# Optimization experiments

Hardware: AMD Instinct MI355X
Metric: run time of the kernel (lower is better)

## Reference

```python
import jax, jax.numpy as jnp
import numpy as np

T, N, E = 4, 4096, 65536
XD, HD, ZD = 256, 256, 64
EPS = 1e-10


def setup_inputs() -> dict:
    key = jax.random.key(0)
    ks = jax.random.split(key, 30)
    rn = lambda k, sh, s=0.05: jax.random.normal(k, sh, dtype=jnp.float32) * s
    inp = {
        "x": rn(ks[0], (T, N, XD), 1.0),
        "edge_idx": jax.random.randint(ks[1], (T, 2, E), 0, N, dtype=jnp.int32),
        "adj": jax.random.bernoulli(ks[2], 0.005, (T, N, N)).astype(jnp.float32),
        "eps_noise": jax.random.normal(ks[3], (T, N, ZD), dtype=jnp.float32),
        "h0": jnp.zeros((1, N, HD), jnp.float32),
        # phi_x / phi_z (Linear+ReLU)
        "phi_x_w": rn(ks[4], (XD, HD)), "phi_x_b": jnp.zeros((HD,), jnp.float32),
        "phi_z_w": rn(ks[5], (ZD, HD)), "phi_z_b": jnp.zeros((HD,), jnp.float32),
        # encoder GCNs
        "enc_w": rn(ks[6], (2 * HD, HD)), "enc_b": jnp.zeros((HD,), jnp.float32),
        "enc_mean_w": rn(ks[7], (HD, ZD)), "enc_mean_b": jnp.zeros((ZD,), jnp.float32),
        "enc_std_w": rn(ks[8], (HD, ZD)), "enc_std_b": jnp.zeros((ZD,), jnp.float32),
        # prior MLPs
        "prior_w": rn(ks[9], (HD, HD)), "prior_b": jnp.zeros((HD,), jnp.float32),
        "prior_mean_w": rn(ks[10], (HD, ZD)), "prior_mean_b": jnp.zeros((ZD,), jnp.float32),
        "prior_std_w": rn(ks[11], (HD, ZD)), "prior_std_b": jnp.zeros((ZD,), jnp.float32),
        # graph-GRU GCNs (bias=False, n_layers=1; x-input is cat[phi_x, phi_z] -> 2*HD)
        "gru_xz_w": rn(ks[12], (2 * HD, HD)), "gru_hz_w": rn(ks[13], (HD, HD)),
        "gru_xr_w": rn(ks[14], (2 * HD, HD)), "gru_hr_w": rn(ks[15], (HD, HD)),
        "gru_xh_w": rn(ks[16], (2 * HD, HD)), "gru_hh_w": rn(ks[17], (HD, HD)),
    }
    return inp


def _gcn(xf, src, dst, W, b):
    """GCNConv: sym-normalized (A + I) aggregation, then bias. Returns pre-activation."""
    h = xf @ W                                             # [N, out]
    deg = 1.0 + jax.ops.segment_sum(jnp.ones(src.shape[0], xf.dtype), dst, num_segments=N)
    dinv = jax.lax.rsqrt(deg)                              # [N]
    norm = dinv[src] * dinv[dst]                           # [E]
    agg = jax.ops.segment_sum(h[src] * norm[:, None], dst, num_segments=N)
    agg = agg + (dinv * dinv)[:, None] * h                 # self-loop term
    if b is not None:
        agg = agg + b
    return agg


def reference(x, edge_idx, adj, eps_noise, h0,
              phi_x_w, phi_x_b, phi_z_w, phi_z_b,
              enc_w, enc_b, enc_mean_w, enc_mean_b, enc_std_w, enc_std_b,
              prior_w, prior_b, prior_mean_w, prior_mean_b, prior_std_w, prior_std_b,
              gru_xz_w, gru_hz_w, gru_xr_w, gru_hr_w, gru_xh_w, gru_hh_w):
    relu, sp, sig = jax.nn.relu, jax.nn.softplus, jax.nn.sigmoid
    h = h0                                                  # [1, N, HD]
    kld = jnp.float32(0.0)
    nll = jnp.float32(0.0)
    enc_means, prior_means = [], []
    nn_f = jnp.float32(N * N)
    for t in range(T):
        src, dst = edge_idx[t, 0], edge_idx[t, 1]
        phi_x_t = relu(x[t] @ phi_x_w + phi_x_b)                       # [N, HD]
        enc_in = jnp.concatenate([phi_x_t, h[-1]], axis=1)             # [N, 2HD]
        enc_t = relu(_gcn(enc_in, src, dst, enc_w, enc_b))
        enc_mean_t = _gcn(enc_t, src, dst, enc_mean_w, enc_mean_b)     # act = identity
        enc_std_t = sp(_gcn(enc_t, src, dst, enc_std_w, enc_std_b))
        prior_t = relu(h[-1] @ prior_w + prior_b)
        prior_mean_t = prior_t @ prior_mean_w + prior_mean_b
        prior_std_t = sp(prior_t @ prior_std_w + prior_std_b)
        z_t = eps_noise[t] * enc_std_t + enc_mean_t                    # reparameterize
        phi_z_t = relu(z_t @ phi_z_w + phi_z_b)
        dec_t = sig(z_t @ z_t.T)                                       # [N, N] decode
        # graph-GRU step (n_layers = 1, bias=False)
        gin = jnp.concatenate([phi_x_t, phi_z_t], axis=1)              # [N, 2HD]
        z_g = sig(_gcn(gin, src, dst, gru_xz_w, None) + _gcn(h[0], src, dst, gru_hz_w, None))
        r_g = sig(_gcn(gin, src, dst, gru_xr_w, None) + _gcn(h[0], src, dst, gru_hr_w, None))
        h_tilde = jnp.tanh(_gcn(gin, src, dst, gru_xh_w, None)
                           + _gcn(r_g * h[0], src, dst, gru_hh_w, None))
        h = (z_g * h[0] + (1.0 - z_g) * h_tilde)[None]                 # [1, N, HD]
        # KLD (faithful to _kld_gauss, including its sign convention)
        s1, s2 = enc_std_t + EPS, prior_std_t + EPS
        kld_el = (2.0 * jnp.log(s2) - 2.0 * jnp.log(s1)
                  - (s1 * s1 + (enc_mean_t - prior_mean_t) ** 2) / (s2 * s2) + 1.0)
        kld = kld + (0.5 / N) * jnp.mean(jnp.sum(kld_el, axis=0))
        # NLL (faithful quirk: BCE-with-logits applied to sigmoid output dec_t)
        a = adj[t]
        tsum = jnp.sum(a)
        posw = (nn_f - tsum) / tsum
        norm = nn_f / ((nn_f - tsum) * 2.0)
        bce = posw * a * sp(-dec_t) + (1.0 - a) * sp(dec_t)
        nll = nll + norm * jnp.mean(bce)
        enc_means.append(enc_mean_t)
        prior_means.append(prior_mean_t)
    return kld, nll, jnp.stack(enc_means), jnp.stack(prior_means), h
```

## Files before the change

kernel.cpp:

```cpp
#include <hip/hip_runtime.h>
#include <hip/hip_bf16.h>

#define T_STEPS 4
#define N 4096
#define E 65536
#define XD 256
#define HD 256
#define ZD 64

typedef __hip_bfloat16 bf16;
typedef __attribute__((ext_vector_type(8))) short short8;
typedef __attribute__((ext_vector_type(4))) float f32x4;

__device__ __forceinline__ float b2f(bf16 v){ return __bfloat162float(v); }
__device__ __forceinline__ bf16 f2b(float v){ return __float2bfloat16(v); }
__device__ __forceinline__ short f2s(float v){ return __builtin_bit_cast(short, f2b(v)); }
__device__ __forceinline__ float bits2f(unsigned int s){ return __builtin_bit_cast(float, s << 16); }
__device__ __forceinline__ float s2f(short s){ return bits2f((unsigned int)(unsigned short)s); }
__device__ __forceinline__ float splus(float x){ return (x > 20.f) ? x : log1pf(expf(x)); }
__device__ __forceinline__ float sigm(float x){ return 1.f/(1.f + expf(-x)); }

__device__ __forceinline__ float ldI(const void* p, size_t i, int f){
  return f ? ((const float*)p)[i] : b2f(((const bf16*)p)[i]);
}
__device__ __forceinline__ void stO(void* p, size_t i, float v, int f){
  if (f) ((float*)p)[i] = v; else ((bf16*)p)[i] = f2b(v);
}
__device__ __forceinline__ void ld8b(const bf16* p, float v[8]){
  uint4 u = *(const uint4*)p;
  v[0]=bits2f(u.x & 0xffffu); v[1]=bits2f(u.x >> 16);
  v[2]=bits2f(u.y & 0xffffu); v[3]=bits2f(u.y >> 16);
  v[4]=bits2f(u.z & 0xffffu); v[5]=bits2f(u.z >> 16);
  v[6]=bits2f(u.w & 0xffffu); v[7]=bits2f(u.w >> 16);
}
__device__ __forceinline__ unsigned int pack2(float a, float b){
  return (unsigned int)(unsigned short)__builtin_bit_cast(unsigned short, f2b(a))
       | ((unsigned int)(unsigned short)__builtin_bit_cast(unsigned short, f2b(b)) << 16);
}

union SMem {
  struct { short As[64*40]; short Wt[64*40]; } g;
  struct { short Zi[64*72]; short Zj[64*72]; short Adj[64*72]; float red[256]; } z;
  struct { float msh[16*128]; } m;
  int sh[256];
  float red[256];
};

struct KP {
  const void *x, *adj, *eps, *h0;
  const int* ei;
  const void *phi_x_w, *phi_x_b, *phi_z_w, *phi_z_b;
  const void *enc_w, *enc_b, *enc_mean_w, *enc_mean_b, *enc_std_w, *enc_std_b;
  const void *prior_w, *prior_b, *prior_mean_w, *prior_mean_b, *prior_std_w, *prior_std_b;
  const void *gxz, *ghz, *gxr, *ghr, *gxh, *ghh;
  void* out;
  float* scal; int* dflag; float* dinv; int* offs; int* srcs; float* enorm; int* deg;
  float* h_prev; bf16* h_bf; bf16* phiXa; bf16* Tb1; bf16* Tb2;
  bf16* zbf; float* z_g; bf16* Gs1; bf16* Gsx; bf16* Gms; bf16* Gh2;
};

#define OUT_EM ((size_t)2)
#define OUT_PM ((size_t)(2 + (size_t)T_STEPS*N*ZD))
#define OUT_H  ((size_t)(2 + (size_t)2*T_STEPS*N*ZD))

__device__ void mfma_tile(SMem& sm, int tid, int f,
    const void* A1, int am1, int lda1, const void* A2, int am2, int lda2,
    int K1, int K, const void* W, int ldw, int wcol,
    const void* bias, int act, bf16* C, int ldc, int row0, int ccol0){
  int ar = tid >> 2, akk = (tid & 3)*8;
  int wk = tid >> 3, wn = (tid & 7)*8;
  int wave = tid >> 6, lane = tid & 63, m = lane & 15, kq = lane >> 4;
  f32x4 acc[4] = {};
  for (int k0 = 0; k0 < K; k0 += 32){
    const void* A; int am, lda, kb;
    if (k0 < K1){ A = A1; am = am1; lda = lda1; kb = k0; }
    else        { A = A2; am = am2; lda = lda2; kb = k0 - K1; }
    size_t aidx = (size_t)(row0 + ar)*lda + kb + akk;
    short8 av;
    if (am == 2 || (am == 1 && f == 0)){
      av = *(const short8*)((const short*)A + aidx);
    } else {
      const float* Af = (const float*)A;
      float4 u0 = *(const float4*)(Af + aidx);
      float4 u1 = *(const float4*)(Af + aidx + 4);
      av[0]=f2s(u0.x); av[1]=f2s(u0.y); av[2]=f2s(u0.z); av[3]=f2s(u0.w);
      av[4]=f2s(u1.x); av[5]=f2s(u1.y); av[6]=f2s(u1.z); av[7]=f2s(u1.w);
    }
    *(short8*)&sm.g.As[ar*40 + akk] = av;
    size_t wi = (size_t)(k0 + wk)*ldw + wcol + wn;
    short wv[8];
    if (f == 0){
      short8 t8 = *(const short8*)((const short*)W + wi);
      #pragma unroll
      for (int j = 0; j < 8; j++) wv[j] = t8[j];
    } else {
      const float* Wf = (const float*)W;
      float4 u0 = *(const float4*)(Wf + wi);
      float4 u1 = *(const float4*)(Wf + wi + 4);
      wv[0]=f2s(u0.x); wv[1]=f2s(u0.y); wv[2]=f2s(u0.z); wv[3]=f2s(u0.w);
      wv[4]=f2s(u1.x); wv[5]=f2s(u1.y); wv[6]=f2s(u1.z); wv[7]=f2s(u1.w);
    }
    #pragma unroll
    for (int j = 0; j < 8; j++){
      int nrow = wn + j;
      int col = (((wk >> 3) ^ ((nrow >> 3) & 3)) << 3) | (wk & 7);
      sm.g.Wt[nrow*40 + col] = wv[j];
    }
    __syncthreads();
    short8 afr = *(const short8*)&sm.g.As[(wave*16 + m)*40 + kq*8];
    #pragma unroll
    for (int t4 = 0; t4 < 4; t4++){
      int nb = t4*16 + m;
      short8 bfr = *(const short8*)&sm.g.Wt[nb*40 + ((kq ^ ((nb >> 3) & 3)) << 3)];
      acc[t4] = __builtin_amdgcn_mfma_f32_16x16x32_bf16(afr, bfr, acc[t4], 0, 0, 0);
    }
    __syncthreads();
  }
  #pragma unroll
  for (int t4 = 0; t4 < 4; t4++){
    int c = ccol0 + t4*16 + m;
    float bv = bias ? ldI(bias, wcol + t4*16 + m, f) : 0.f;
    #pragma unroll
    for (int reg = 0; reg < 4; reg++){
      int r = row0 + wave*16 + kq*4 + reg;
      float v = acc[t4][reg] + bv;
      if (act == 1) v = fmaxf(v, 0.f);
      C[(size_t)r*ldc + c] = f2b(v);
    }
  }
}

__device__ void dec_tile1(const KP& p, SMem& sm, int tid, int t, int u, int f){
  int i0 = (u >> 6)*64, j0 = (u & 63)*64;
  size_t aoff = (size_t)t*N*N;
  #pragma unroll
  for (int i = 0; i < 2; i++){
    int idx = tid + i*256;
    int r = idx >> 3, c = idx & 7;
    int col = ((c ^ ((r >> 3) & 3)) << 3);
    *(short8*)&sm.z.Zi[r*72 + col] = *(const short8*)((const short*)p.zbf + (size_t)(i0+r)*ZD + c*8);
    *(short8*)&sm.z.Zj[r*72 + col] = *(const short8*)((const short*)p.zbf + (size_t)(j0+r)*ZD + c*8);
  }
  {
    int row = tid >> 2, c0 = (tid & 3)*16;
    if (f){
      const float* ap = (const float*)p.adj + aoff + (size_t)(i0+row)*N + j0 + c0;
      short tmp[16];
      #pragma unroll
      for (int q = 0; q < 16; q += 4){
        float4 v = *(const float4*)(ap + q);
        tmp[q]=f2s(v.x); tmp[q+1]=f2s(v.y); tmp[q+2]=f2s(v.z); tmp[q+3]=f2s(v.w);
      }
      *(short8*)&sm.z.Adj[row*72 + c0]     = *(short8*)&tmp[0];
      *(short8*)&sm.z.Adj[row*72 + c0 + 8] = *(short8*)&tmp[8];
    } else {
      const short* ap = (const short*)p.adj + aoff + (size_t)(i0+row)*N + j0 + c0;
      *(short8*)&sm.z.Adj[row*72 + c0]     = *(const short8*)ap;
      *(short8*)&sm.z.Adj[row*72 + c0 + 8] = *(const short8*)(ap + 8);
    }
  }
  __syncthreads();
  int wave = tid >> 6, lane = tid & 63, m = lane & 15, kq = lane >> 4;
  int ra = wave*16 + m, sa = (ra >> 3) & 3;
  short8 a1 = *(const short8*)&sm.z.Zi[ra*72 + ((kq ^ sa) << 3)];
  short8 a2 = *(const short8*)&sm.z.Zi[ra*72 + (((kq+4) ^ sa) << 3)];
  f32x4 acc[4] = {};
  #pragma unroll
  for (int t4 = 0; t4 < 4; t4++){
    int rb = t4*16 + m, sb2 = (rb >> 3) & 3;
    short8 b1 = *(const short8*)&sm.z.Zj[rb*72 + ((kq ^ sb2) << 3)];
    short8 b2 = *(const short8*)&sm.z.Zj[rb*72 + (((kq+4) ^ sb2) << 3)];
    acc[t4] = __builtin_amdgcn_mfma_f32_16x16x32_bf16(a1, b1, acc[t4], 0, 0, 0);
    acc[t4] = __builtin_amdgcn_mfma_f32_16x16x32_bf16(a2, b2, acc[t4], 0, 0, 0);
  }
  float lts = 0.f, lP = 0.f, lQ = 0.f;
  #pragma unroll
  for (int t4 = 0; t4 < 4; t4++){
    int lj = t4*16 + m;
    #pragma unroll
    for (int reg = 0; reg < 4; reg++){
      int li = wave*16 + kq*4 + reg;
      float av = s2f(sm.z.Adj[li*72 + lj]);
      float dec = sigm(acc[t4][reg]);
      lts += av;
      lQ += (1.f - av)*log1pf(expf(dec));
      if (av != 0.f) lP += av*log1pf(expf(-dec));
    }
  }
  __syncthreads();
  sm.z.red[tid] = lts; __syncthreads();
  for (int o = 128; o > 0; o >>= 1){ if (tid < o) sm.z.red[tid] += sm.z.red[tid+o]; __syncthreads(); }
  if (tid == 0) atomicAdd(p.scal + 8 + t, sm.z.red[0]);
  __syncthreads();
  sm.z.red[tid] = lP; __syncthreads();
  for (int o = 128; o > 0; o >>= 1){ if (tid < o) sm.z.red[tid] += sm.z.red[tid+o]; __syncthreads(); }
  if (tid == 0) atomicAdd(p.scal + 12 + t, sm.z.red[0]);
  __syncthreads();
  sm.z.red[tid] = lQ; __syncthreads();
  for (int o = 128; o > 0; o >>= 1){ if (tid < o) sm.z.red[tid] += sm.z.red[tid+o]; __syncthreads(); }
  if (tid == 0) atomicAdd(p.scal + 16 + t, sm.z.red[0]);
}

__global__ __launch_bounds__(256) void setup0_k(KP p){
  int gb = blockIdx.x, tid = threadIdx.x;
  if (gb == 0){ if (tid < 64) p.scal[tid] = 0.f; }
  else if (gb == 1){
    if (tid == 0){
      const unsigned short* u = (const unsigned short*)p.x;
      int big = 0;
      for (int i = 0; i < 256; i++){ int e = (u[i] >> 7) & 0xFF; if (e >= 134) big++; }
      *p.dflag = (big > 16) ? 1 : 0;
    }
  } else {
    p.deg[(gb-2)*256 + tid] = 0;
  }
}

__global__ __launch_bounds__(256) void count_deg_k(KP p){
  int idx = blockIdx.x*256 + threadIdx.x;
  int t = idx >> 16, e = idx & (E-1);
  int dst = p.ei[(size_t)t*2*E + E + e] & (N-1);
  atomicAdd(&p.deg[t*N + dst], 1);
}

__global__ __launch_bounds__(256) void setup2_k(KP p){
  __shared__ SMem sm;
  int gb = blockIdx.x, tid = threadIdx.x;
  int f = *p.dflag;
  if (gb < 4){
    int t = gb;
    const int* dg = p.deg + t*N;
    int* of = p.offs + t*(N+1);
    int base = tid*16;
    int loc[16]; int s = 0;
    #pragma unroll
    for (int i = 0; i < 16; i++){ loc[i] = s; s += dg[base+i]; }
    sm.sh[tid] = s;
    __syncthreads();
    for (int o = 1; o < 256; o <<= 1){
      int v = (tid >= o) ? sm.sh[tid-o] : 0;
      __syncthreads();
      sm.sh[tid] += v;
      __syncthreads();
    }
    int pre = (tid == 0) ? 0 : sm.sh[tid-1];
    #pragma unroll
    for (int i = 0; i < 16; i++){
      int deg_i = dg[base+i];
      of[base+i] = pre + loc[i];
      p.dinv[t*N + base + i] = rsqrtf(1.f + (float)deg_i);
    }
    if (tid == 255) of[N] = sm.sh[255];
    __syncthreads();
    #pragma unroll
    for (int i = 0; i < 16; i++) p.deg[t*N + base + i] = pre + loc[i];
  } else if (gb < 36){
    for (int idx = (gb-4)*256 + tid; idx < N*HD; idx += 32*256){
      float v = ldI(p.h0, idx, f);
      p.h_prev[idx] = v; p.h_bf[idx] = f2b(v);
    }
  } else {
    for (int u = gb - 36; u < 1024; u += 988){
      int colblk = u & 3, rowblk = u >> 2;
      mfma_tile(sm, tid, f, p.x, 1, XD, nullptr, 0, 0, XD, XD,
                p.phi_x_w, HD, colblk*64, p.phi_x_b, 1,
                p.phiXa, HD, rowblk*64, colblk*64);
    }
  }
}

__global__ __launch_bounds__(256) void scatter_k(KP p){
  int idx = blockIdx.x*256 + threadIdx.x;
  int t = idx >> 16, e = idx & (E-1);
  int s = p.ei[(size_t)t*2*E + e] & (N-1);
  int d = p.ei[(size_t)t*2*E + E + e] & (N-1);
  int pos = atomicAdd(&p.deg[t*N + d], 1);
  if (pos >= 0 && pos < E){
    p.srcs[(size_t)t*E + pos] = s;
    p.enorm[(size_t)t*E + pos] = p.dinv[t*N + s] * p.dinv[t*N + d];
  }
}

__global__ __launch_bounds__(256) void g1_k(KP p, int t){
  __shared__ SMem sm;
  int gb = blockIdx.x, tid = threadIdx.x, f = *p.dflag;
  const bf16* phiX = p.phiXa + (size_t)t*N*HD;
  int colblk = gb & 15, rowblk = gb >> 4;
  int grp = colblk >> 2, c4 = colblk & 3;
  if (grp == 0)
    mfma_tile(sm, tid, f, phiX, 2, HD, p.h_bf, 2, HD, 256, 512,
              p.enc_w, HD, c4*64, nullptr, 0, p.Gs1, 1024, rowblk*64, colblk*64);
  else if (grp == 1)
    mfma_tile(sm, tid, f, p.h_bf, 2, HD, nullptr, 0, 0, 256, 256,
              p.prior_w, HD, c4*64, p.prior_b, 1, p.Gs1, 1024, rowblk*64, colblk*64);
  else if (grp == 2)
    mfma_tile(sm, tid, f, p.h_bf, 2, HD, nullptr, 0, 0, 256, 256,
              p.ghz, HD, c4*64, nullptr, 0, p.Gs1, 1024, rowblk*64, colblk*64);
  else
    mfma_tile(sm, tid, f, p.h_bf, 2, HD, nullptr, 0, 0, 256, 256,
              p.ghr, HD, c4*64, nullptr, 0, p.Gs1, 1024, rowblk*64, colblk*64);
}

__global__ __launch_bounds__(256) void encagg_pms_k(KP p, int t){
  __shared__ SMem sm;
  int gb = blockIdx.x, tid = threadIdx.x, f = *p.dflag;
  const int* offs_t = p.offs + t*(N+1);
  const int* srcs_t = p.srcs + (size_t)t*E;
  const float* en_t = p.enorm + (size_t)t*E;
  const float* dv_t = p.dinv + t*N;
  if (gb < 512){
    int g8 = tid >> 5, l = tid & 31;
    int n = gb*8 + g8, c = l*8;
    int e0 = offs_t[n], e1 = offs_t[n+1];
    float d2 = dv_t[n]*dv_t[n];
    float acc[8], v[8];
    ld8b(p.Gs1 + (size_t)n*1024 + c, v);
    #pragma unroll
    for (int j = 0; j < 8; j++) acc[j] = d2 * v[j];
    for (int e = e0; e < e1; e++){
      int s = srcs_t[e] & (N-1);
      float nm = en_t[e];
      ld8b(p.Gs1 + (size_t)s*1024 + c, v);
      #pragma unroll
      for (int j = 0; j < 8; j++) acc[j] += nm * v[j];
    }
    #pragma unroll
    for (int j = 0; j < 8; j++) acc[j] = fmaxf(acc[j] + ldI(p.enc_b, c + j, f), 0.f);
    uint4 o; o.x = pack2(acc[0],acc[1]); o.y = pack2(acc[2],acc[3]);
    o.z = pack2(acc[4],acc[5]); o.w = pack2(acc[6],acc[7]);
    *(uint4*)(p.Tb1 + (size_t)n*HD + c) = o;
  } else {
    int u = gb - 512;
    int colblk = u & 1, rowblk = u >> 1;
    mfma_tile(sm, tid, f, p.Gs1 + 256, 2, 1024, nullptr, 0, 0, 256, 256,
              colblk ? p.prior_std_w : p.prior_mean_w, ZD, 0,
              colblk ? p.prior_std_b : p.prior_mean_b, 0,
              p.Gms, 256, rowblk*64, 128 + colblk*64);
  }
}

__global__ __launch_bounds__(256) void encms_k(KP p, int t){
  __shared__ SMem sm;
  int gb = blockIdx.x, tid = threadIdx.x, f = *p.dflag;
  int colblk = gb & 1, rowblk = gb >> 1;
  mfma_tile(sm, tid, f, p.Tb1, 2, HD, nullptr, 0, 0, 256, 256,
            colblk ? p.enc_std_w : p.enc_mean_w, ZD, 0, nullptr, 0,
            p.Gms, 256, rowblk*64, colblk*64);
}

__global__ __launch_bounds__(256) void msaggpost_k(KP p, int t){
  __shared__ SMem sm;
  int gb = blockIdx.x, tid = threadIdx.x, f = *p.dflag;
  const int* offs_t = p.offs + t*(N+1);
  const int* srcs_t = p.srcs + (size_t)t*E;
  const float* en_t = p.enorm + (size_t)t*E;
  const float* dv_t = p.dinv + t*N;
  int g16 = tid >> 4, l = tid & 15;
  int n = gb*16 + g16, c = l*8;
  {
    int e0 = offs_t[n], e1 = offs_t[n+1];
    float d2 = dv_t[n]*dv_t[n];
    float acc[8], v[8];
    ld8b(p.Gms + (size_t)n*256 + c, v);
    #pragma unroll
    for (int j = 0; j < 8; j++) acc[j] = d2 * v[j];
    for (int e = e0; e < e1; e++){
      int s = srcs_t[e] & (N-1);
      float nm = en_t[e];
      ld8b(p.Gms + (size_t)s*256 + c, v);
      #pragma unroll
      for (int j = 0; j < 8; j++) acc[j] += nm * v[j];
    }
    #pragma unroll
    for (int j = 0; j < 8; j++) sm.m.msh[g16*128 + c + j] = acc[j];
  }
  __syncthreads();
  float el = 0.f;
  {
    int d0 = l*4;
    #pragma unroll
    for (int q = 0; q < 4; q++){
      int d = d0 + q;
      size_t idx = (size_t)n*ZD + d;
      float mean = sm.m.msh[g16*128 + d] + ldI(p.enc_mean_b, d, f);
      float sd = splus(sm.m.msh[g16*128 + 64 + d] + ldI(p.enc_std_b, d, f));
      float zv = ldI(p.eps, (size_t)t*N*ZD + idx, f) * sd + mean;
      p.zbf[idx] = f2b(zv);
      stO(p.out, OUT_EM + (size_t)t*N*ZD + idx, mean, f);
      float pm = b2f(p.Gms[(size_t)n*256 + 128 + d]);
      float ps = splus(b2f(p.Gms[(size_t)n*256 + 192 + d]));
      stO(p.out, OUT_PM + (size_t)t*N*ZD + idx, pm, f);
      float s1 = sd + 1e-10f, s2 = ps + 1e-10f;
      float dm = mean - pm;
      el += 2.f*(logf(s2) - logf(s1)) - (s1*s1 + dm*dm)/(s2*s2) + 1.f;
    }
  }
  __syncthreads();
  sm.red[tid] = el; __syncthreads();
  for (int o = 128; o > 0; o >>= 1){ if (tid < o) sm.red[tid] += sm.red[tid+o]; __syncthreads(); }
  if (tid == 0) atomicAdd(p.scal + 4, sm.red[0] * (0.5f/((float)N*(float)ZD)));
}

__global__ __launch_bounds__(256) void phiz_k(KP p, int t){
  __shared__ SMem sm;
  int gb = blockIdx.x, tid = threadIdx.x, f = *p.dflag;
  int colblk = gb & 3, rowblk = gb >> 2;
  mfma_tile(sm, tid, f, p.zbf, 2, ZD, nullptr, 0, 0, ZD, ZD,
            p.phi_z_w, HD, colblk*64, p.phi_z_b, 1, p.Tb2, HD, rowblk*64, colblk*64);
}

__global__ __launch_bounds__(256) void grux_dec_k(KP p, int t){
  __shared__ SMem sm;
  int gb = blockIdx.x, tid = threadIdx.x, f = *p.dflag;
  if (gb < 768){
    const bf16* phiX = p.phiXa + (size_t)t*N*HD;
    int colblk = gb % 12, rowblk = gb / 12;
    int grp = colblk >> 2, c4 = colblk & 3;
    const void* W = (grp == 0) ? p.gxz : ((grp == 1) ? p.gxr : p.gxh);
    mfma_tile(sm, tid, f, phiX, 2, HD, p.Tb2, 2, HD, 256, 512,
              W, HD, c4*64, nullptr, 0, p.Gsx, 768, rowblk*64, colblk*64);
  } else {
    dec_tile1(p, sm, tid, t, gb - 768, f);
  }
}

__global__ __launch_bounds__(256) void zr_k(KP p, int t){
  int gb = blockIdx.x, tid = threadIdx.x;
  const int* offs_t = p.offs + t*(N+1);
  const int* srcs_t = p.srcs + (size_t)t*E;
  const float* en_t = p.enorm + (size_t)t*E;
  const float* dv_t = p.dinv + t*N;
  int g4 = tid >> 6, lane = tid & 63;
  int n = gb*4 + g4, c = lane*8;
  int e0 = offs_t[n], e1 = offs_t[n+1];
  float d2 = dv_t[n]*dv_t[n];
  float acc[8], v1[8], v2[8];
  ld8b(p.Gsx + (size_t)n*768 + c, v1);
  ld8b(p.Gs1 + 512 + (size_t)n*1024 + c, v2);
  #pragma unroll
  for (int j = 0; j < 8; j++) acc[j] = d2 * (v1[j] + v2[j]);
  for (int e = e0; e < e1; e++){
    int s = srcs_t[e] & (N-1);
    float nm = en_t[e];
    ld8b(p.Gsx + (size_t)s*768 + c, v1);
    ld8b(p.Gs1 + 512 + (size_t)s*1024 + c, v2);
    #pragma unroll
    for (int j = 0; j < 8; j++) acc[j] += nm * (v1[j] + v2[j]);
  }
  if (c < 256){
    size_t base = (size_t)n*HD + c;
    float4 o0, o1;
    o0.x = sigm(acc[0]); o0.y = sigm(acc[1]); o0.z = sigm(acc[2]); o0.w = sigm(acc[3]);
    o1.x = sigm(acc[4]); o1.y = sigm(acc[5]); o1.z = sigm(acc[6]); o1.w = sigm(acc[7]);
    *(float4*)(p.z_g + base) = o0;
    *(float4*)(p.z_g + base + 4) = o1;
  } else {
    size_t base = (size_t)n*HD + (c - 256);
    float r[8];
    #pragma unroll
    for (int j = 0; j < 8; j++) r[j] = sigm(acc[j]) * p.h_prev[base+j];
    uint4 o; o.x = pack2(r[0],r[1]); o.y = pack2(r[2],r[3]);
    o.z = pack2(r[4],r[5]); o.w = pack2(r[6],r[7]);
    *(uint4*)(p.Tb1 + base) = o;
  }
}

__global__ __launch_bounds__(256) void hh_k(KP p, int t){
  __shared__ SMem sm;
  int gb = blockIdx.x, tid = threadIdx.x, f = *p.dflag;
  int colblk = gb & 3, rowblk = gb >> 2;
  mfma_tile(sm, tid, f, p.Tb1, 2, HD, nullptr, 0, 0, 256, 256,
            p.ghh, HD, colblk*64, nullptr, 0, p.Gh2, 256, rowblk*64, colblk*64);
}

__global__ __launch_bounds__(256) void hagg_k(KP p, int t){
  int gb = blockIdx.x, tid = threadIdx.x, f = *p.dflag;
  const int* offs_t = p.offs + t*(N+1);
  const int* srcs_t = p.srcs + (size_t)t*E;
  const float* en_t = p.enorm + (size_t)t*E;
  const float* dv_t = p.dinv + t*N;
  int g8 = tid >> 5, l = tid & 31;
  int n = gb*8 + g8, c = l*8;
  int e0 = offs_t[n], e1 = offs_t[n+1];
  float d2 = dv_t[n]*dv_t[n];
  float acc[8], v1[8], v2[8];
  ld8b(p.Gsx + 512 + (size_t)n*768 + c, v1);
  ld8b(p.Gh2 + (size_t)n*256 + c, v2);
  #pragma unroll
  for (int j = 0; j < 8; j++) acc[j] = d2 * (v1[j] + v2[j]);
  for (int e = e0; e < e1; e++){
    int s = srcs_t[e] & (N-1);
    float nm = en_t[e];
    ld8b(p.Gsx + 512 + (size_t)s*768 + c, v1);
    ld8b(p.Gh2 + (size_t)s*256 + c, v2);
    #pragma unroll
    for (int j = 0; j < 8; j++) acc[j] += nm * (v1[j] + v2[j]);
  }
  size_t base = (size_t)n*HD + c;
  #pragma unroll
  for (int j = 0; j < 8; j++){
    float z = p.z_g[base+j];
    float hv = p.h_prev[base+j];
    float nv = z*hv + (1.f - z)*tanhf(acc[j]);
    p.h_prev[base+j] = nv;
    p.h_bf[base+j] = f2b(nv);
    if (t == T_STEPS-1) stO(p.out, OUT_H + base + j, nv, f);
  }
}

__global__ void fin_k(KP p){
  if (threadIdx.x == 0){
    int f = *p.dflag;
    const float NNf = 16777216.f;
    float nll = 0.f;
    for (int t = 0; t < T_STEPS; t++){
      float ts = p.scal[8+t], P = p.scal[12+t], Q = p.scal[16+t];
      float posw = (NNf - ts)/ts;
      nll += (posw*P + Q) * 0.5f/(NNf - ts);
    }
    stO(p.out, 0, p.scal[4], f);
    stO(p.out, 1, nll, f);
  }
}

extern "C" void kernel_launch(void* const* d_in, const int* in_sizes, int n_in,
                              void* d_out, int out_size, void* d_ws, size_t ws_size,
                              hipStream_t stream){
  KP P;
  P.x = d_in[0];  P.ei = (const int*)d_in[1];  P.adj = d_in[2];  P.eps = d_in[3];  P.h0 = d_in[4];
  P.phi_x_w = d_in[5];  P.phi_x_b = d_in[6];  P.phi_z_w = d_in[7];  P.phi_z_b = d_in[8];
  P.enc_w = d_in[9];  P.enc_b = d_in[10];
  P.enc_mean_w = d_in[11];  P.enc_mean_b = d_in[12];
  P.enc_std_w = d_in[13];   P.enc_std_b = d_in[14];
  P.prior_w = d_in[15];  P.prior_b = d_in[16];
  P.prior_mean_w = d_in[17];  P.prior_mean_b = d_in[18];
  P.prior_std_w = d_in[19];   P.prior_std_b = d_in[20];
  P.gxz = d_in[21];  P.ghz = d_in[22];  P.gxr = d_in[23];
  P.ghr = d_in[24];  P.gxh = d_in[25];  P.ghh = d_in[26];
  P.out = d_out;

  char* wp = (char*)d_ws;
  auto alloc = [&](size_t bytes){ void* q = (void*)wp; wp += (bytes + 255) & ~(size_t)255; return q; };
  P.scal  = (float*)alloc(64*sizeof(float));
  P.dflag = (int*)  alloc(256);
  P.dinv  = (float*)alloc((size_t)T_STEPS*N*4);
  P.offs  = (int*)  alloc((size_t)T_STEPS*(N+1)*4);
  P.srcs  = (int*)  alloc((size_t)T_STEPS*E*4);
  P.enorm = (float*)alloc((size_t)T_STEPS*E*4);
  P.deg   = (int*)  alloc((size_t)T_STEPS*N*4);
  P.h_prev= (float*)alloc((size_t)N*HD*4);
  P.h_bf  = (bf16*) alloc((size_t)N*HD*2);
  P.phiXa = (bf16*) alloc((size_t)T_STEPS*N*HD*2);
  P.Tb1   = (bf16*) alloc((size_t)N*HD*2);
  P.Tb2   = (bf16*) alloc((size_t)N*HD*2);
  P.zbf   = (bf16*) alloc((size_t)N*ZD*2);
  P.z_g   = (float*)alloc((size_t)N*HD*4);
  P.Gs1   = (bf16*) alloc((size_t)N*1024*2);
  P.Gsx   = (bf16*) alloc((size_t)N*768*2);
  P.Gms   = (bf16*) alloc((size_t)N*256*2);
  P.Gh2   = (bf16*) alloc((size_t)N*256*2);

  setup0_k<<<66,256,0,stream>>>(P);
  count_deg_k<<<1024,256,0,stream>>>(P);
  setup2_k<<<1024,256,0,stream>>>(P);
  scatter_k<<<1024,256,0,stream>>>(P);
  for (int t = 0; t < T_STEPS; t++){
    g1_k<<<1024,256,0,stream>>>(P, t);
    encagg_pms_k<<<640,256,0,stream>>>(P, t);
    encms_k<<<128,256,0,stream>>>(P, t);
    msaggpost_k<<<256,256,0,stream>>>(P, t);
    phiz_k<<<256,256,0,stream>>>(P, t);
    grux_dec_k<<<4864,256,0,stream>>>(P, t);
    zr_k<<<1024,256,0,stream>>>(P, t);
    hh_k<<<256,256,0,stream>>>(P, t);
    hagg_k<<<512,256,0,stream>>>(P, t);
  }
  fin_k<<<1,64,0,stream>>>(P);
}
```

Before: 1.546 ms.

## Fold scatter and final kernels into neighbors, unroll gathers, use fast math

Folds the edge-scatter kernel into the first g1_k launch as extra blocks, and folds the final loss kernel into the last hagg_k launch as an extra block. This removes two launches. Neighbor-gather loops are unrolled by two edges so more loads are in flight at once, and the three block reductions are merged into one pass with fewer barriers. Exact softplus, sigmoid, tanh and log are replaced by fast __expf/__logf approximations, which lowers precision slightly. The msh shared-memory stride is padded to 132.

```diff
diff --git a/kernel.cpp b/kernel.cpp
--- a/kernel.cpp
+++ b/kernel.cpp
@@ -17,8 +17,9 @@
 __device__ __forceinline__ short f2s(float v){ return __builtin_bit_cast(short, f2b(v)); }
 __device__ __forceinline__ float bits2f(unsigned int s){ return __builtin_bit_cast(float, s << 16); }
 __device__ __forceinline__ float s2f(short s){ return bits2f((unsigned int)(unsigned short)s); }
-__device__ __forceinline__ float splus(float x){ return (x > 20.f) ? x : log1pf(expf(x)); }
-__device__ __forceinline__ float sigm(float x){ return 1.f/(1.f + expf(-x)); }
+__device__ __forceinline__ float splus(float x){ return (x > 15.f) ? x : __logf(1.f + __expf(x)); }
+__device__ __forceinline__ float sigm(float x){ return 1.f/(1.f + __expf(-x)); }
+__device__ __forceinline__ float ftanh(float x){ return 2.f/(1.f + __expf(-2.f*x)) - 1.f; }
 
 __device__ __forceinline__ float ldI(const void* p, size_t i, int f){
   return f ? ((const float*)p)[i] : b2f(((const bf16*)p)[i]);
@@ -33,15 +34,29 @@
   v[4]=bits2f(u.z & 0xffffu); v[5]=bits2f(u.z >> 16);
   v[6]=bits2f(u.w & 0xffffu); v[7]=bits2f(u.w >> 16);
 }
+__device__ __forceinline__ void ldW8(const void* W, size_t off, int f, float w[8]){
+  if (f == 0){ ld8b((const bf16*)W + off, w); }
+  else {
+    const float* Wf = (const float*)W + off;
+    float4 a = *(const float4*)Wf, b = *(const float4*)(Wf + 4);
+    w[0]=a.x; w[1]=a.y; w[2]=a.z; w[3]=a.w; w[4]=b.x; w[5]=b.y; w[6]=b.z; w[7]=b.w;
+  }
+}
 __device__ __forceinline__ unsigned int pack2(float a, float b){
   return (unsigned int)(unsigned short)__builtin_bit_cast(unsigned short, f2b(a))
        | ((unsigned int)(unsigned short)__builtin_bit_cast(unsigned short, f2b(b)) << 16);
 }
+__device__ __forceinline__ uint4 pack8(const float v[8]){
+  uint4 o; o.x = pack2(v[0],v[1]); o.y = pack2(v[2],v[3]);
+  o.z = pack2(v[4],v[5]); o.w = pack2(v[6],v[7]);
+  return o;
+}
 
 union SMem {
   struct { short As[64*40]; short Wt[64*40]; } g;
-  struct { short Zi[64*72]; short Zj[64*72]; short Adj[64*72]; float red[256]; } z;
-  struct { float msh[16*128]; } m;
+  struct { short Zi[64*72]; short Zj[64*72]; short Adj[64*72];
+           float redA[256]; float redB[256]; float redC[256]; } z;
+  struct { float msh[16*132]; } m;
   int sh[256];
   float red[256];
 };
@@ -88,17 +103,15 @@
     }
     *(short8*)&sm.g.As[ar*40 + akk] = av;
     size_t wi = (size_t)(k0 + wk)*ldw + wcol + wn;
-    short wv[8];
+    float wf[8]; short wv[8];
     if (f == 0){
       short8 t8 = *(const short8*)((const short*)W + wi);
       #pragma unroll
       for (int j = 0; j < 8; j++) wv[j] = t8[j];
     } else {
-      const float* Wf = (const float*)W;
-      float4 u0 = *(const float4*)(Wf + wi);
-      float4 u1 = *(const float4*)(Wf + wi + 4);
-      wv[0]=f2s(u0.x); wv[1]=f2s(u0.y); wv[2]=f2s(u0.z); wv[3]=f2s(u0.w);
-      wv[4]=f2s(u1.x); wv[5]=f2s(u1.y); wv[6]=f2s(u1.z); wv[7]=f2s(u1.w);
+      ldW8(W, wi, f, wf);
+      #pragma unroll
+      for (int j = 0; j < 8; j++) wv[j] = f2s(wf[j]);
     }
     #pragma unroll
     for (int j = 0; j < 8; j++){
@@ -183,22 +196,26 @@
       float av = s2f(sm.z.Adj[li*72 + lj]);
       float dec = sigm(acc[t4][reg]);
       lts += av;
-      lQ += (1.f - av)*log1pf(expf(dec));
-      if (av != 0.f) lP += av*log1pf(expf(-dec));
+      lQ += (1.f - av)*splus(dec);
+      if (av != 0.f) lP += av*splus(-dec);
     }
   }
   __syncthreads();
-  sm.z.red[tid] = lts; __syncthreads();
-  for (int o = 128; o > 0; o >>= 1){ if (tid < o) sm.z.red[tid] += sm.z.red[tid+o]; __syncthreads(); }
-  if (tid == 0) atomicAdd(p.scal + 8 + t, sm.z.red[0]);
+  sm.z.redA[tid] = lts; sm.z.redB[tid] = lP; sm.z.redC[tid] = lQ;
   __syncthreads();
-  sm.z.red[tid] = lP; __syncthreads();
-  for (int o = 128; o > 0; o >>= 1){ if (tid < o) sm.z.red[tid] += sm.z.red[tid+o]; __syncthreads(); }
-  if (tid == 0) atomicAdd(p.scal + 12 + t, sm.z.red[0]);
-  __syncthreads();
-  sm.z.red[tid] = lQ; __syncthreads();
-  for (int o = 128; o > 0; o >>= 1){ if (tid < o) sm.z.red[tid] += sm.z.red[tid+o]; __syncthreads(); }
-  if (tid == 0) atomicAdd(p.scal + 16 + t, sm.z.red[0]);
+  for (int o = 128; o > 0; o >>= 1){
+    if (tid < o){
+      sm.z.redA[tid] += sm.z.redA[tid+o];
+      sm.z.redB[tid] += sm.z.redB[tid+o];
+      sm.z.redC[tid] += sm.z.redC[tid+o];
+    }
+    __syncthreads();
+  }
+  if (tid == 0){
+    atomicAdd(p.scal + 8 + t,  sm.z.redA[0]);
+    atomicAdd(p.scal + 12 + t, sm.z.redB[0]);
+    atomicAdd(p.scal + 16 + t, sm.z.redC[0]);
+  }
 }
 
 __global__ __launch_bounds__(256) void setup0_k(KP p){
@@ -260,30 +277,29 @@
       p.h_prev[idx] = v; p.h_bf[idx] = f2b(v);
     }
   } else {
-    for (int u = gb - 36; u < 1024; u += 988){
-      int colblk = u & 3, rowblk = u >> 2;
-      mfma_tile(sm, tid, f, p.x, 1, XD, nullptr, 0, 0, XD, XD,
-                p.phi_x_w, HD, colblk*64, p.phi_x_b, 1,
-                p.phiXa, HD, rowblk*64, colblk*64);
-    }
-  }
-}
-
-__global__ __launch_bounds__(256) void scatter_k(KP p){
-  int idx = blockIdx.x*256 + threadIdx.x;
-  int t = idx >> 16, e = idx & (E-1);
-  int s = p.ei[(size_t)t*2*E + e] & (N-1);
-  int d = p.ei[(size_t)t*2*E + E + e] & (N-1);
-  int pos = atomicAdd(&p.deg[t*N + d], 1);
-  if (pos >= 0 && pos < E){
-    p.srcs[(size_t)t*E + pos] = s;
-    p.enorm[(size_t)t*E + pos] = p.dinv[t*N + s] * p.dinv[t*N + d];
+    int u = gb - 36;
+    int colblk = u & 3, rowblk = u >> 2;
+    mfma_tile(sm, tid, f, p.x, 1, XD, nullptr, 0, 0, XD, XD,
+              p.phi_x_w, HD, colblk*64, p.phi_x_b, 1,
+              p.phiXa, HD, rowblk*64, colblk*64);
   }
 }
 
 __global__ __launch_bounds__(256) void g1_k(KP p, int t){
   __shared__ SMem sm;
   int gb = blockIdx.x, tid = threadIdx.x, f = *p.dflag;
+  if (gb >= 1024){
+    int idx = (gb - 1024)*256 + tid;
+    int tt = idx >> 16, e = idx & (E-1);
+    int s = p.ei[(size_t)tt*2*E + e] & (N-1);
+    int d = p.ei[(size_t)tt*2*E + E + e] & (N-1);
+    int pos = atomicAdd(&p.deg[tt*N + d], 1);
+    if (pos >= 0 && pos < E){
+      p.srcs[(size_t)tt*E + pos] = s;
+      p.enorm[(size_t)tt*E + pos] = p.dinv[tt*N + s] * p.dinv[tt*N + d];
+    }
+    return;
+  }
   const bf16* phiX = p.phiXa + (size_t)t*N*HD;
   int colblk = gb & 15, rowblk = gb >> 4;
   int grp = colblk >> 2, c4 = colblk & 3;
@@ -313,22 +329,29 @@
     int n = gb*8 + g8, c = l*8;
     int e0 = offs_t[n], e1 = offs_t[n+1];
     float d2 = dv_t[n]*dv_t[n];
-    float acc[8], v[8];
-    ld8b(p.Gs1 + (size_t)n*1024 + c, v);
-    #pragma unroll
-    for (int j = 0; j < 8; j++) acc[j] = d2 * v[j];
-    for (int e = e0; e < e1; e++){
-      int s = srcs_t[e] & (N-1);
-      float nm = en_t[e];
-      ld8b(p.Gs1 + (size_t)s*1024 + c, v);
+    float acc[8], va[8], vb[8];
+    ld8b(p.Gs1 + (size_t)n*1024 + c, va);
+    #pragma unroll
+    for (int j = 0; j < 8; j++) acc[j] = d2 * va[j];
+    int e = e0;
+    for (; e + 1 < e1; e += 2){
+      int s0 = srcs_t[e] & (N-1), s1 = srcs_t[e+1] & (N-1);
+      float n0 = en_t[e], n1 = en_t[e+1];
+      ld8b(p.Gs1 + (size_t)s0*1024 + c, va);
+      ld8b(p.Gs1 + (size_t)s1*1024 + c, vb);
       #pragma unroll
-      for (int j = 0; j < 8; j++) acc[j] += nm * v[j];
+      for (int j = 0; j < 8; j++) acc[j] += n0*va[j] + n1*vb[j];
+    }
+    if (e < e1){
+      int s0 = srcs_t[e] & (N-1);
+      float n0 = en_t[e];
+      ld8b(p.Gs1 + (size_t)s0*1024 + c, va);
+      #pragma unroll
+      for (int j = 0; j < 8; j++) acc[j] += n0*va[j];
     }
     #pragma unroll
     for (int j = 0; j < 8; j++) acc[j] = fmaxf(acc[j] + ldI(p.enc_b, c + j, f), 0.f);
-    uint4 o; o.x = pack2(acc[0],acc[1]); o.y = pack2(acc[2],acc[3]);
-    o.z = pack2(acc[4],acc[5]); o.w = pack2(acc[6],acc[7]);
-    *(uint4*)(p.Tb1 + (size_t)n*HD + c) = o;
+    *(uint4*)(p.Tb1 + (size_t)n*HD + c) = pack8(acc);
   } else {
     int u = gb - 512;
     int colblk = u & 1, rowblk = u >> 1;
@@ -360,19 +383,28 @@
   {
     int e0 = offs_t[n], e1 = offs_t[n+1];
     float d2 = dv_t[n]*dv_t[n];
-    float acc[8], v[8];
-    ld8b(p.Gms + (size_t)n*256 + c, v);
-    #pragma unroll
-    for (int j = 0; j < 8; j++) acc[j] = d2 * v[j];
-    for (int e = e0; e < e1; e++){
-      int s = srcs_t[e] & (N-1);
-      float nm = en_t[e];
-      ld8b(p.Gms + (size_t)s*256 + c, v);
+    float acc[8], va[8], vb[8];
+    ld8b(p.Gms + (size_t)n*256 + c, va);
+    #pragma unroll
+    for (int j = 0; j < 8; j++) acc[j] = d2 * va[j];
+    int e = e0;
+    for (; e + 1 < e1; e += 2){
+      int s0 = srcs_t[e] & (N-1), s1 = srcs_t[e+1] & (N-1);
+      float n0 = en_t[e], n1 = en_t[e+1];
+      ld8b(p.Gms + (size_t)s0*256 + c, va);
+      ld8b(p.Gms + (size_t)s1*256 + c, vb);
       #pragma unroll
-      for (int j = 0; j < 8; j++) acc[j] += nm * v[j];
-    }
-    #pragma unroll
-    for (int j = 0; j < 8; j++) sm.m.msh[g16*128 + c + j] = acc[j];
+      for (int j = 0; j < 8; j++) acc[j] += n0*va[j] + n1*vb[j];
+    }
+    if (e < e1){
+      int s0 = srcs_t[e] & (N-1);
+      float n0 = en_t[e];
+      ld8b(p.Gms + (size_t)s0*256 + c, va);
+      #pragma unroll
+      for (int j = 0; j < 8; j++) acc[j] += n0*va[j];
+    }
+    #pragma unroll
+    for (int j = 0; j < 8; j++) sm.m.msh[g16*132 + c + j] = acc[j];
   }
   __syncthreads();
   float el = 0.f;
@@ -382,9 +414,9 @@
     for (int q = 0; q < 4; q++){
       int d = d0 + q;
       size_t idx = (size_t)n*ZD + d;
-      float mean = sm.m.msh[g16*128 + d] + ldI(p.enc_mean_b, d, f);
-      float sd = splus(sm.m.msh[g16*128 + 64 + d] + ldI(p.enc_std_b, d, f));
-      float zv = ldI(p.eps, (size_t)t*N*ZD + idx, f) * sd + mean;
+      float mean = sm.m.msh[g16*132 + d] + ldI(p.enc_mean_b, d, f);
+      float sd = splus(sm.m.msh[g16*132 + 64 + d] + ldI(p.enc_std_b, d, f));
+      float zv = ldI(p.eps, (size_t)t*N*ZD + idx, f)*sd + mean;
       p.zbf[idx] = f2b(zv);
       stO(p.out, OUT_EM + (size_t)t*N*ZD + idx, mean, f);
       float pm = b2f(p.Gms[(size_t)n*256 + 128 + d]);
@@ -392,7 +424,7 @@
       stO(p.out, OUT_PM + (size_t)t*N*ZD + idx, pm, f);
       float s1 = sd + 1e-10f, s2 = ps + 1e-10f;
       float dm = mean - pm;
-      el += 2.f*(logf(s2) - logf(s1)) - (s1*s1 + dm*dm)/(s2*s2) + 1.f;
+      el += 2.f*(__logf(s2) - __logf(s1)) - (s1*s1 + dm*dm)/(s2*s2) + 1.f;
     }
   }
   __syncthreads();
@@ -434,18 +466,29 @@
   int n = gb*4 + g4, c = lane*8;
   int e0 = offs_t[n], e1 = offs_t[n+1];
   float d2 = dv_t[n]*dv_t[n];
-  float acc[8], v1[8], v2[8];
+  float acc[8], v1[8], v2[8], v3[8], v4[8];
   ld8b(p.Gsx + (size_t)n*768 + c, v1);
   ld8b(p.Gs1 + 512 + (size_t)n*1024 + c, v2);
   #pragma unroll
   for (int j = 0; j < 8; j++) acc[j] = d2 * (v1[j] + v2[j]);
-  for (int e = e0; e < e1; e++){
-    int s = srcs_t[e] & (N-1);
-    float nm = en_t[e];
-    ld8b(p.Gsx + (size_t)s*768 + c, v1);
-    ld8b(p.Gs1 + 512 + (size_t)s*1024 + c, v2);
-    #pragma unroll
-    for (int j = 0; j < 8; j++) acc[j] += nm * (v1[j] + v2[j]);
+  int e = e0;
+  for (; e + 1 < e1; e += 2){
+    int s0 = srcs_t[e] & (N-1), s1 = srcs_t[e+1] & (N-1);
+    float n0 = en_t[e], n1 = en_t[e+1];
+    ld8b(p.Gsx + (size_t)s0*768 + c, v1);
+    ld8b(p.Gs1 + 512 + (size_t)s0*1024 + c, v2);
+    ld8b(p.Gsx + (size_t)s1*768 + c, v3);
+    ld8b(p.Gs1 + 512 + (size_t)s1*1024 + c, v4);
+    #pragma unroll
+    for (int j = 0; j < 8; j++) acc[j] += n0*(v1[j] + v2[j]) + n1*(v3[j] + v4[j]);
+  }
+  if (e < e1){
+    int s0 = srcs_t[e] & (N-1);
+    float n0 = en_t[e];
+    ld8b(p.Gsx + (size_t)s0*768 + c, v1);
+    ld8b(p.Gs1 + 512 + (size_t)s0*1024 + c, v2);
+    #pragma unroll
+    for (int j = 0; j < 8; j++) acc[j] += n0*(v1[j] + v2[j]);
   }
   if (c < 256){
     size_t base = (size_t)n*HD + c;
@@ -459,9 +502,7 @@
     float r[8];
     #pragma unroll
     for (int j = 0; j < 8; j++) r[j] = sigm(acc[j]) * p.h_prev[base+j];
-    uint4 o; o.x = pack2(r[0],r[1]); o.y = pack2(r[2],r[3]);
-    o.z = pack2(r[4],r[5]); o.w = pack2(r[6],r[7]);
-    *(uint4*)(p.Tb1 + base) = o;
+    *(uint4*)(p.Tb1 + base) = pack8(r);
   }
 }
 
@@ -475,6 +516,20 @@
 
 __global__ __launch_bounds__(256) void hagg_k(KP p, int t){
   int gb = blockIdx.x, tid = threadIdx.x, f = *p.dflag;
+  if (gb >= 512){
+    if (tid == 0){
+      const float NNf = 16777216.f;
+      float nll = 0.f;
+      for (int tt = 0; tt < T_STEPS; tt++){
+        float ts = p.scal[8+tt], P = p.scal[12+tt], Q = p.scal[16+tt];
+        float posw = (NNf - ts)/ts;
+        nll += (posw*P + Q) * 0.5f/(NNf - ts);
+      }
+      stO(p.out, 0, p.scal[4], f);
+      stO(p.out, 1, nll, f);
+    }
+    return;
+  }
   const int* offs_t = p.offs + t*(N+1);
   const int* srcs_t = p.srcs + (size_t)t*E;
   const float* en_t = p.enorm + (size_t)t*E;
@@ -483,43 +538,39 @@
   int n = gb*8 + g8, c = l*8;
   int e0 = offs_t[n], e1 = offs_t[n+1];
   float d2 = dv_t[n]*dv_t[n];
-  float acc[8], v1[8], v2[8];
+  float acc[8], v1[8], v2[8], v3[8], v4[8];
   ld8b(p.Gsx + 512 + (size_t)n*768 + c, v1);
   ld8b(p.Gh2 + (size_t)n*256 + c, v2);
   #pragma unroll
   for (int j = 0; j < 8; j++) acc[j] = d2 * (v1[j] + v2[j]);
-  for (int e = e0; e < e1; e++){
-    int s = srcs_t[e] & (N-1);
-    float nm = en_t[e];
-    ld8b(p.Gsx + 512 + (size_t)s*768 + c, v1);
-    ld8b(p.Gh2 + (size_t)s*256 + c, v2);
-    #pragma unroll
-    for (int j = 0; j < 8; j++) acc[j] += nm * (v1[j] + v2[j]);
+  int e = e0;
+  for (; e + 1 < e1; e += 2){
+    int s0 = srcs_t[e] & (N-1), s1 = srcs_t[e+1] & (N-1);
+    float n0 = en_t[e], n1 = en_t[e+1];
+    ld8b(p.Gsx + 512 + (size_t)s0*768 + c, v1);
+    ld8b(p.Gh2 + (size_t)s0*256 + c, v2);
+    ld8b(p.Gsx + 512 + (size_t)s1*768 + c, v3);
+    ld8b(p.Gh2 + (size_t)s1*256 + c, v4);
+    #pragma unroll
+    for (int j = 0; j < 8; j++) acc[j] += n0*(v1[j] + v2[j]) + n1*(v3[j] + v4[j]);
+  }
+  if (e < e1){
+    int s0 = srcs_t[e] & (N-1);
+    float n0 = en_t[e];
+    ld8b(p.Gsx + 512 + (size_t)s0*768 + c, v1);
+    ld8b(p.Gh2 + (size_t)s0*256 + c, v2);
+    #pragma unroll
+    for (int j = 0; j < 8; j++) acc[j] += n0*(v1[j] + v2[j]);
   }
   size_t base = (size_t)n*HD + c;
   #pragma unroll
   for (int j = 0; j < 8; j++){
     float z = p.z_g[base+j];
     float hv = p.h_prev[base+j];
-    float nv = z*hv + (1.f - z)*tanhf(acc[j]);
+    float nv = z*hv + (1.f - z)*ftanh(acc[j]);
     p.h_prev[base+j] = nv;
     p.h_bf[base+j] = f2b(nv);
     if (t == T_STEPS-1) stO(p.out, OUT_H + base + j, nv, f);
-  }
-}
-
-__global__ void fin_k(KP p){
-  if (threadIdx.x == 0){
-    int f = *p.dflag;
-    const float NNf = 16777216.f;
-    float nll = 0.f;
-    for (int t = 0; t < T_STEPS; t++){
-      float ts = p.scal[8+t], P = p.scal[12+t], Q = p.scal[16+t];
-      float posw = (NNf - ts)/ts;
-      nll += (posw*P + Q) * 0.5f/(NNf - ts);
-    }
-    stO(p.out, 0, p.scal[4], f);
-    stO(p.out, 1, nll, f);
   }
 }
 
@@ -562,10 +613,9 @@
 
   setup0_k<<<66,256,0,stream>>>(P);
   count_deg_k<<<1024,256,0,stream>>>(P);
-  setup2_k<<<1024,256,0,stream>>>(P);
-  scatter_k<<<1024,256,0,stream>>>(P);
+  setup2_k<<<1060,256,0,stream>>>(P);
   for (int t = 0; t < T_STEPS; t++){
-    g1_k<<<1024,256,0,stream>>>(P, t);
+    g1_k<<<(t == 0) ? 2048 : 1024,256,0,stream>>>(P, t);
     encagg_pms_k<<<640,256,0,stream>>>(P, t);
     encms_k<<<128,256,0,stream>>>(P, t);
     msaggpost_k<<<256,256,0,stream>>>(P, t);
@@ -573,7 +623,6 @@
     grux_dec_k<<<4864,256,0,stream>>>(P, t);
     zr_k<<<1024,256,0,stream>>>(P, t);
     hh_k<<<256,256,0,stream>>>(P, t);
-    hagg_k<<<512,256,0,stream>>>(P, t);
-  }
-  fin_k<<<1,64,0,stream>>>(P);
-}
+    hagg_k<<<(t == T_STEPS-1) ? 513 : 512,256,0,stream>>>(P, t);
+  }
+}
```

Result: faster. 1.404 ms (-9.1%).
